# Kernel tuning notes

Measured on AMD Instinct MI355X. Metric: run time of the kernel, lower is better.

The kernel has to match this reference:

```python
import jax, jax.numpy as jnp
import numpy as np

N_TARGET = 1_000_000
GRID = 220
C_IN, C_OUT = 32, 64
BN_EPS = 1e-5


def _build_topology():
    # Real sparse-voxel topology: random occupied cells in a GRID^3 volume.
    rng = np.random.default_rng(0)
    raw = rng.integers(0, GRID, size=(1_400_000, 3), dtype=np.int64)
    keys = np.unique((raw[:, 0] * GRID + raw[:, 1]) * GRID + raw[:, 2])[:N_TARGET]
    N = keys.shape[0]
    coords = np.stack([keys // (GRID * GRID), (keys // GRID) % GRID, keys % GRID], axis=1)
    # Rulebook: for each of the 27 kernel offsets, index of the neighbor voxel (N = missing -> zero pad row).
    nbr = np.full((N, 27), N, dtype=np.int32)
    k = 0
    for dx in (-1, 0, 1):
        for dy in (-1, 0, 1):
            for dz in (-1, 0, 1):
                nc = coords + np.array([dx, dy, dz])
                valid = np.all((nc >= 0) & (nc < GRID), axis=1)
                nk = (nc[:, 0] * GRID + nc[:, 1]) * GRID + nc[:, 2]
                pos = np.clip(np.searchsorted(keys, nk), 0, N - 1)
                found = valid & (keys[pos] == nk)
                nbr[found, k] = pos[found].astype(np.int32)
                k += 1
    # MaxPool(2,2): voxels sharing coords//2 pool together.
    PG = GRID // 2 + 1
    pkeys = ((coords[:, 0] // 2) * PG + coords[:, 1] // 2) * PG + coords[:, 2] // 2
    uniq, pool_ids = np.unique(pkeys, return_inverse=True)
    return N, nbr, pool_ids.astype(np.int32), int(uniq.shape[0])


def setup_inputs() -> dict:
    N, nbr, pool_ids, num_pooled = _build_topology()
    key = jax.random.key(0)
    k1, k2, k3 = jax.random.split(key, 3)
    return {
        "feats": jax.random.normal(k1, (N, C_IN), dtype=jnp.float32),
        "W1": jax.random.normal(k2, (27, C_IN, C_OUT), dtype=jnp.float32) * 0.1,
        "gamma1": jnp.ones((C_OUT,), jnp.float32),
        "beta1": jnp.zeros((C_OUT,), jnp.float32),
        "W2": jax.random.normal(k3, (27, C_OUT, C_OUT), dtype=jnp.float32) * 0.1,
        "gamma2": jnp.ones((C_OUT,), jnp.float32),
        "beta2": jnp.zeros((C_OUT,), jnp.float32),
        "nbr_idx": jnp.asarray(nbr),
        "pool_ids": jnp.asarray(pool_ids),
        "num_pooled": num_pooled,
    }


def _sparse_conv3(f, W, nbr_idx):
    # f: [N, Cin], W: [27, Cin, Cout], nbr_idx: [N, 27] with pad index N.
    N = f.shape[0]
    fp = jnp.concatenate([f, jnp.zeros((1, f.shape[1]), f.dtype)], axis=0)  # zero pad row
    out = jnp.zeros((N, W.shape[2]), f.dtype)
    for k in range(27):  # fixed kernel offsets: gather -> GEMM -> accumulate
        out = out + fp[nbr_idx[:, k]] @ W[k]
    return out


def _batch_norm(f, gamma, beta):
    # Training-mode BN over the voxel dim (biased variance), as torch BatchNorm.
    m = f.mean(axis=0)
    v = f.var(axis=0)
    return (f - m) * jax.lax.rsqrt(v + BN_EPS) * gamma + beta


def reference(feats, W1, gamma1, beta1, W2, gamma2, beta2, nbr_idx, pool_ids, num_pooled):
    x = jax.nn.relu(_batch_norm(_sparse_conv3(feats, W1, nbr_idx), gamma1, beta1))
    x = _batch_norm(_sparse_conv3(x, W2, nbr_idx), gamma2, beta2)
    pooled = jax.ops.segment_max(x, pool_ids, num_segments=num_pooled)
    return x, pooled
```

## Files before the change

kernel.cpp:

```cpp
#include <hip/hip_runtime.h>
#include <hip/hip_bf16.h>
#include <stdint.h>

#define TPB 256

typedef __bf16 bf16x8 __attribute__((ext_vector_type(8)));
typedef float f32x4 __attribute__((ext_vector_type(4)));
union U16x8 { uint4 u; bf16x8 b; };

typedef const uint32_t __attribute__((address_space(1))) glb_u32;
typedef uint32_t __attribute__((address_space(3))) lds_u32;

__device__ __forceinline__ uint16_t f2bf_rne(float f) {
  union { float f; uint32_t u; } c; c.f = f;
  uint32_t r = 0x7FFFu + ((c.u >> 16) & 1u);
  return (uint16_t)((c.u + r) >> 16);
}

__global__ __launch_bounds__(TPB) void prep_w_kernel(
    const float* __restrict__ W1, const float* __restrict__ W2,
    uint16_t* __restrict__ w1t, uint16_t* __restrict__ w2t)
{
  int i = blockIdx.x * TPB + threadIdx.x;
  if (i < 27 * 2048) {
    int k = i >> 11, cin = (i >> 6) & 31, cout = i & 63;
    int cin2 = (((cin >> 3) ^ (cout & 3)) << 3) | (cin & 7);
    w1t[(k << 11) + (cout << 5) + cin2] = f2bf_rne(W1[i]);
  } else {
    int j = i - 27 * 2048;
    if (j < 27 * 4096) {
      int k = j >> 12, cin = (j >> 6) & 63, cout = j & 63;
      int cin2 = (((cin >> 3) ^ (cout & 7)) << 3) | (cin & 7);
      w2t[(k << 12) + (cout << 6) + cin2] = f2bf_rne(W2[j]);
    }
  }
}

__global__ __launch_bounds__(TPB) void prep_x0_kernel(
    const float* __restrict__ feats, uint16_t* __restrict__ x0, long long N)
{
  long long t = (long long)blockIdx.x * TPB + threadIdx.x;
  if (t >= (N + 1) * 4) return;
  long long e = t * 8;
  uint4 o;
  if (e < N * 32) {
    float4 a = *(const float4*)(feats + e);
    float4 b = *(const float4*)(feats + e + 4);
    o.x = (uint32_t)f2bf_rne(a.x) | ((uint32_t)f2bf_rne(a.y) << 16);
    o.y = (uint32_t)f2bf_rne(a.z) | ((uint32_t)f2bf_rne(a.w) << 16);
    o.z = (uint32_t)f2bf_rne(b.x) | ((uint32_t)f2bf_rne(b.y) << 16);
    o.w = (uint32_t)f2bf_rne(b.z) | ((uint32_t)f2bf_rne(b.w) << 16);
  } else {
    o.x = o.y = o.z = o.w = 0;
  }
  *(uint4*)(x0 + e) = o;
}

__global__ __launch_bounds__(TPB) void bucket_build_kernel(
    const int* __restrict__ pool_ids, int* __restrict__ count,
    int* __restrict__ members, long long N)
{
  long long i = (long long)blockIdx.x * TPB + threadIdx.x;
  if (i < N) {
    int pid = pool_ids[i];
    int slot = atomicAdd(&count[pid], 1);
    members[(long long)pid * 8 + slot] = (int)i;
  }
}

template <int CIN, int R>
__global__ __launch_bounds__(TPB, 2) void conv_mfma_kernel(
    const uint16_t* __restrict__ x, const uint16_t* __restrict__ wt,
    const int* __restrict__ nbr, float* __restrict__ y,
    float* __restrict__ statsrep, int N)
{
  constexpr int CHUNKS = CIN / 32;
  constexpr int LOGROWB = (CIN == 32) ? 6 : 7;
  constexpr int SWZ = (CIN == 32) ? 3 : 7;
  constexpr int WKB = 64 * CIN * 2;
  constexpr int NISSUE = WKB / (TPB * 16);
  constexpr int ROWS = 4 * R * 16;
  constexpr int NINTS = ROWS * 27;
  constexpr int NCH16 = NINTS / 4;

  __shared__ __align__(16) char Wlds[2][WKB];
  __shared__ __align__(16) int nbrLds[NINTS];
  __shared__ float sred[4][128];

  const int tid = threadIdx.x;
  const int lane = tid & 63;
  const int wave = tid >> 6;
  const int l15 = lane & 15;
  const int l4 = lane >> 4;
  const long long row0 = (long long)blockIdx.x * ROWS;

  f32x4 acc[R][4];
#pragma unroll
  for (int r = 0; r < R; ++r)
#pragma unroll
    for (int t = 0; t < 4; ++t)
      acc[r][t] = (f32x4){0.f, 0.f, 0.f, 0.f};

  {
    const char* nsrc = (const char*)nbr + row0 * 108;
    long long blkB = (long long)N * 108 - row0 * 108;
    int fullChunks = (int)(blkB >> 4);
    if (fullChunks > NCH16) fullChunks = NCH16;
#pragma unroll
    for (int u = 0; u < (NCH16 + TPB - 1) / TPB; ++u) {
      int idx = u * TPB + tid;
      if (idx < fullChunks)
        __builtin_amdgcn_global_load_lds((glb_u32*)(nsrc + idx * 16),
                                         (lds_u32*)((char*)nbrLds + idx * 16), 16, 0, 0);
    }
    for (int ii = fullChunks * 4 + tid; ii < NINTS; ii += TPB) {
      long long gi = row0 * 27 + ii;
      nbrLds[ii] = (gi < (long long)N * 27) ? nbr[gi] : N;
    }
  }

  auto stageW = [&](int k, int b) {
    const char* src = (const char*)(wt + (size_t)k * 64 * CIN);
#pragma unroll
    for (int u = 0; u < NISSUE; ++u) {
      int off = (tid + u * TPB) * 16;
      __builtin_amdgcn_global_load_lds((glb_u32*)(src + off),
                                       (lds_u32*)(&Wlds[b][off]), 16, 0, 0);
    }
  };
  auto gather = [&](int k, U16x8 (&dst)[R][CHUNKS]) {
#pragma unroll
    for (int r = 0; r < R; ++r) {
      int lrow = (wave * R + r) * 16 + l15;
      int g = nbrLds[lrow * 27 + k];
      const uint16_t* xr = x + (size_t)g * CIN + (l4 << 3);
#pragma unroll
      for (int c = 0; c < CHUNKS; ++c)
        dst[r][c].u = *(const uint4*)(xr + c * 32);
    }
  };
  auto compute = [&](int wsel, U16x8 (&xs)[R][CHUNKS]) {
    bf16x8 bfrag[4][CHUNKS];
#pragma unroll
    for (int t = 0; t < 4; ++t) {
      int n = t * 16 + l15;
#pragma unroll
      for (int c = 0; c < CHUNKS; ++c) {
        int colb = (l4 << 4) + (c << 6);
        int d = (n << LOGROWB) | (colb ^ ((n & SWZ) << 4));
        U16x8 tmp; tmp.u = *(const uint4*)(&Wlds[wsel][d]);
        bfrag[t][c] = tmp.b;
      }
    }
#pragma unroll
    for (int r = 0; r < R; ++r)
#pragma unroll
      for (int c = 0; c < CHUNKS; ++c)
#pragma unroll
        for (int t = 0; t < 4; ++t)
          acc[r][t] = __builtin_amdgcn_mfma_f32_16x16x32_bf16(
              xs[r][c].b, bfrag[t][c], acc[r][t], 0, 0, 0);
  };

  U16x8 xA[R][CHUNKS], xB[R][CHUNKS];

  stageW(0, 0);
  __syncthreads();
  gather(0, xA);

#pragma unroll 1
  for (int kk = 0; kk < 13; ++kk) {
    if (kk > 0) __syncthreads();
    stageW(2 * kk + 1, 1);
    gather(2 * kk + 1, xB);
    compute(0, xA);
    __syncthreads();
    if (2 * kk + 2 < 27) {
      stageW(2 * kk + 2, 0);
      gather(2 * kk + 2, xA);
    }
    compute(1, xB);
  }
  __syncthreads();
  compute(0, xA);

#pragma unroll
  for (int r = 0; r < R; ++r) {
    long long vr0 = row0 + (wave * R + r) * 16 + (l4 << 2);
#pragma unroll
    for (int reg = 0; reg < 4; ++reg) {
      long long vr = vr0 + reg;
      if (vr < N) {
        float* yr = y + vr * 64 + l15;
#pragma unroll
        for (int t = 0; t < 4; ++t) yr[t * 16] = acc[r][t][reg];
      }
    }
  }

  float s[4], s2[4];
#pragma unroll
  for (int t = 0; t < 4; ++t) { s[t] = 0.f; s2[t] = 0.f; }
#pragma unroll
  for (int r = 0; r < R; ++r) {
    long long vr0 = row0 + (wave * R + r) * 16 + (l4 << 2);
#pragma unroll
    for (int reg = 0; reg < 4; ++reg) {
      if (vr0 + reg < N) {
#pragma unroll
        for (int t = 0; t < 4; ++t) {
          float v = acc[r][t][reg];
          s[t] += v;
          s2[t] = fmaf(v, v, s2[t]);
        }
      }
    }
  }
#pragma unroll
  for (int t = 0; t < 4; ++t) {
    s[t] += __shfl_xor(s[t], 16);
    s[t] += __shfl_xor(s[t], 32);
    s2[t] += __shfl_xor(s2[t], 16);
    s2[t] += __shfl_xor(s2[t], 32);
  }
  __syncthreads();
  if (l4 == 0) {
#pragma unroll
    for (int t = 0; t < 4; ++t) {
      sred[wave][t * 16 + l15] = s[t];
      sred[wave][64 + t * 16 + l15] = s2[t];
    }
  }
  __syncthreads();
  if (tid < 128) {
    float tot = sred[0][tid] + sred[1][tid] + sred[2][tid] + sred[3][tid];
    atomicAdd(&statsrep[(blockIdx.x & 15) * 128 + tid], tot);
  }
}

__global__ void bn_finalize_kernel(const float* __restrict__ reps,
                                   float* __restrict__ fin, float n)
{
  int c = threadIdx.x;
  float s = 0.f, s2 = 0.f;
  for (int r = 0; r < 16; ++r) { s += reps[r * 128 + c]; s2 += reps[r * 128 + 64 + c]; }
  float mean = s / n;
  float var = s2 / n - mean * mean;
  fin[c] = mean;
  fin[64 + c] = rsqrtf(var + 1e-5f);
}

__global__ __launch_bounds__(TPB) void bn_relu_bf16_kernel(
    const float* __restrict__ y, const float* __restrict__ fin,
    const float* __restrict__ gamma, const float* __restrict__ beta,
    uint16_t* __restrict__ x1, long long N)
{
  long long e = ((long long)blockIdx.x * TPB + threadIdx.x) * 4;
  if (e >= (N + 1) * 64) return;
  long long row = e >> 6;
  int c = (int)(e & 63);
  ushort4 out;
  if (row < N) {
    float4 v = *(const float4*)(y + e);
    float4 m = *(const float4*)(fin + c);
    float4 r = *(const float4*)(fin + 64 + c);
    float4 g = *(const float4*)(gamma + c);
    float4 b = *(const float4*)(beta + c);
    float o0 = fmaf((v.x - m.x) * r.x, g.x, b.x);
    float o1 = fmaf((v.y - m.y) * r.y, g.y, b.y);
    float o2 = fmaf((v.z - m.z) * r.z, g.z, b.z);
    float o3 = fmaf((v.w - m.w) * r.w, g.w, b.w);
    o0 = o0 > 0.f ? o0 : 0.f; o1 = o1 > 0.f ? o1 : 0.f;
    o2 = o2 > 0.f ? o2 : 0.f; o3 = o3 > 0.f ? o3 : 0.f;
    out.x = f2bf_rne(o0); out.y = f2bf_rne(o1); out.z = f2bf_rne(o2); out.w = f2bf_rne(o3);
  } else {
    out.x = 0; out.y = 0; out.z = 0; out.w = 0;
  }
  *(ushort4*)(x1 + e) = out;
}

__global__ __launch_bounds__(TPB) void pool_max_kernel(
    const float* __restrict__ y, const float* __restrict__ fin,
    const float* __restrict__ gamma, const float* __restrict__ beta,
    const int* __restrict__ count, const int* __restrict__ members,
    float* __restrict__ pooled, long long P)
{
  long long pid = (long long)blockIdx.x * 16 + (threadIdx.x >> 4);
  if (pid >= P) return;
  int c0 = (threadIdx.x & 15) * 4;
  float4 m = *(const float4*)(fin + c0);
  float4 r = *(const float4*)(fin + 64 + c0);
  float4 g = *(const float4*)(gamma + c0);
  float4 b = *(const float4*)(beta + c0);
  int cnt = count[pid];
  float4 acc = {-3.4e38f, -3.4e38f, -3.4e38f, -3.4e38f};
  const int* mem = members + pid * 8;
  for (int t = 0; t < cnt; ++t) {
    long long row = mem[t];
    float4 v = *(const float4*)(y + row * 64 + c0);
    acc.x = fmaxf(acc.x, fmaf((v.x - m.x) * r.x, g.x, b.x));
    acc.y = fmaxf(acc.y, fmaf((v.y - m.y) * r.y, g.y, b.y));
    acc.z = fmaxf(acc.z, fmaf((v.z - m.z) * r.z, g.z, b.z));
    acc.w = fmaxf(acc.w, fmaf((v.w - m.w) * r.w, g.w, b.w));
  }
  *(float4*)(pooled + pid * 64 + c0) = acc;
}

__global__ __launch_bounds__(TPB) void bn_write_kernel(
    const float* __restrict__ y, const float* __restrict__ fin,
    const float* __restrict__ gamma, const float* __restrict__ beta,
    float* __restrict__ xout, long long N)
{
  long long e = ((long long)blockIdx.x * TPB + threadIdx.x) * 4;
  if (e >= N * 64) return;
  int c = (int)(e & 63);
  float4 v = *(const float4*)(y + e);
  float4 m = *(const float4*)(fin + c);
  float4 r = *(const float4*)(fin + 64 + c);
  float4 g = *(const float4*)(gamma + c);
  float4 b = *(const float4*)(beta + c);
  float4 o;
  o.x = fmaf((v.x - m.x) * r.x, g.x, b.x);
  o.y = fmaf((v.y - m.y) * r.y, g.y, b.y);
  o.z = fmaf((v.z - m.z) * r.z, g.z, b.z);
  o.w = fmaf((v.w - m.w) * r.w, g.w, b.w);
  *(float4*)(xout + e) = o;
}

extern "C" void kernel_launch(void* const* d_in, const int* in_sizes, int n_in,
                              void* d_out, int out_size, void* d_ws, size_t ws_size,
                              hipStream_t stream)
{
  const float* feats  = (const float*)d_in[0];
  const float* W1     = (const float*)d_in[1];
  const float* gamma1 = (const float*)d_in[2];
  const float* beta1  = (const float*)d_in[3];
  const float* W2     = (const float*)d_in[4];
  const float* gamma2 = (const float*)d_in[5];
  const float* beta2  = (const float*)d_in[6];
  const int* nbr      = (const int*)d_in[7];
  const int* pool_ids = (const int*)d_in[8];

  const long long N = (long long)in_sizes[0] / 32;
  const long long P = (long long)out_size / 64 - N;

  char* ws = (char*)d_ws;
  float* y = (float*)ws;
  size_t y_bytes = (size_t)N * 64 * 4;
  char* regB = ws + y_bytes;
  size_t regB_bytes = ((size_t)(N + 1) * 64 * 2 + 255) & ~(size_t)255;
  uint16_t* x0 = (uint16_t*)regB;
  uint16_t* x1 = (uint16_t*)regB;
  float* reps1 = (float*)(regB + regB_bytes);
  float* reps2 = reps1 + 16 * 128;
  float* fin1 = reps2 + 16 * 128;
  float* fin2 = fin1 + 128;

  float* xout = (float*)d_out;
  float* pooled = xout + (size_t)N * 64;
  int* count   = (int*)xout;
  int* members = count + P;
  uint16_t* w1t = (uint16_t*)pooled;
  uint16_t* w2t = w1t + 27 * 2048;

  hipMemsetAsync(reps1, 0, 2 * 16 * 128 * sizeof(float), stream);
  hipMemsetAsync(count, 0, (size_t)P * 4, stream);

  prep_w_kernel<<<(27 * 2048 + 27 * 4096 + TPB - 1) / TPB, TPB, 0, stream>>>(W1, W2, w1t, w2t);
  prep_x0_kernel<<<(int)(((N + 1) * 4 + TPB - 1) / TPB), TPB, 0, stream>>>(feats, x0, N);
  bucket_build_kernel<<<(int)((N + TPB - 1) / TPB), TPB, 0, stream>>>(pool_ids, count, members, N);

  const int convBlocks = (int)((N + 255) / 256);
  conv_mfma_kernel<32, 4><<<convBlocks, TPB, 0, stream>>>(x0, w1t, nbr, y, reps1, (int)N);
  bn_finalize_kernel<<<1, 64, 0, stream>>>(reps1, fin1, (float)N);

  long long e1 = ((N + 1) * 64) / 4;
  bn_relu_bf16_kernel<<<(int)((e1 + TPB - 1) / TPB), TPB, 0, stream>>>(
      y, fin1, gamma1, beta1, x1, N);

  conv_mfma_kernel<64, 4><<<convBlocks, TPB, 0, stream>>>(x1, w2t, nbr, y, reps2, (int)N);
  bn_finalize_kernel<<<1, 64, 0, stream>>>(reps2, fin2, (float)N);

  pool_max_kernel<<<(int)((P + 15) / 16), TPB, 0, stream>>>(
      y, fin2, gamma2, beta2, count, members, pooled, P);

  long long e2 = (N * 64) / 4;
  bn_write_kernel<<<(int)((e2 + TPB - 1) / TPB), TPB, 0, stream>>>(
      y, fin2, gamma2, beta2, xout, N);
}
```

Before: 758.9 us.

## Deepen conv pipeline with explicit vmcnt barriers, XCD-aware block remap, higher occupancy

Restructures the conv main loop so both weight buffers and both gather register sets are prefetched before the loop. Each stage then waits on a partial vmcnt plus a raw s_barrier instead of __syncthreads, with sched_barriers fencing the code, so gathers for the next offset stay in flight during MFMA compute. Block IDs are remapped so consecutive row ranges land on the same XCD for better L2 locality. Launch-bounds occupancy rises to 4 and 3 waves-per-SIMD targets, which risks register spills or correctness problems if the vmcnt count does not match the outstanding LDS-direct loads.

```diff
diff --git a/kernel.cpp b/kernel.cpp
--- a/kernel.cpp
+++ b/kernel.cpp
@@ -10,6 +10,16 @@
 
 typedef const uint32_t __attribute__((address_space(1))) glb_u32;
 typedef uint32_t __attribute__((address_space(3))) lds_u32;
+
+template <int N> __device__ __forceinline__ void wait_barrier() {
+  __builtin_amdgcn_sched_barrier(0);
+  asm volatile("s_waitcnt vmcnt(%0)" :: "i"(N) : "memory");
+  __builtin_amdgcn_s_barrier();
+  __builtin_amdgcn_sched_barrier(0);
+}
+__device__ __forceinline__ void fence_sched() {
+  __builtin_amdgcn_sched_barrier(0);
+}
 
 __device__ __forceinline__ uint16_t f2bf_rne(float f) {
   union { float f; uint32_t u; } c; c.f = f;
@@ -68,8 +78,8 @@
   }
 }
 
-template <int CIN, int R>
-__global__ __launch_bounds__(TPB, 2) void conv_mfma_kernel(
+template <int CIN, int R, int OCC>
+__global__ __launch_bounds__(TPB, OCC) void conv_mfma_kernel(
     const uint16_t* __restrict__ x, const uint16_t* __restrict__ wt,
     const int* __restrict__ nbr, float* __restrict__ y,
     float* __restrict__ statsrep, int N)
@@ -78,7 +88,8 @@
   constexpr int LOGROWB = (CIN == 32) ? 6 : 7;
   constexpr int SWZ = (CIN == 32) ? 3 : 7;
   constexpr int WKB = 64 * CIN * 2;
-  constexpr int NISSUE = WKB / (TPB * 16);
+  constexpr int NW = WKB / (TPB * 16);
+  constexpr int NG = R * CHUNKS;
   constexpr int ROWS = 4 * R * 16;
   constexpr int NINTS = ROWS * 27;
   constexpr int NCH16 = NINTS / 4;
@@ -92,7 +103,14 @@
   const int wave = tid >> 6;
   const int l15 = lane & 15;
   const int l4 = lane >> 4;
-  const long long row0 = (long long)blockIdx.x * ROWS;
+
+  int bid;
+  {
+    int nwg = gridDim.x, q = nwg >> 3, r = nwg & 7;
+    int xcd = blockIdx.x & 7, pos = blockIdx.x >> 3;
+    bid = (xcd < r ? xcd * (q + 1) : r * (q + 1) + (xcd - r) * q) + pos;
+  }
+  const long long row0 = (long long)bid * ROWS;
 
   f32x4 acc[R][4];
 #pragma unroll
@@ -122,7 +140,7 @@
   auto stageW = [&](int k, int b) {
     const char* src = (const char*)(wt + (size_t)k * 64 * CIN);
 #pragma unroll
-    for (int u = 0; u < NISSUE; ++u) {
+    for (int u = 0; u < NW; ++u) {
       int off = (tid + u * TPB) * 16;
       __builtin_amdgcn_global_load_lds((glb_u32*)(src + off),
                                        (lds_u32*)(&Wlds[b][off]), 16, 0, 0);
@@ -165,23 +183,29 @@
   U16x8 xA[R][CHUNKS], xB[R][CHUNKS];
 
   stageW(0, 0);
+  stageW(1, 1);
   __syncthreads();
   gather(0, xA);
+  gather(1, xB);
+  fence_sched();
 
 #pragma unroll 1
   for (int kk = 0; kk < 13; ++kk) {
-    if (kk > 0) __syncthreads();
-    stageW(2 * kk + 1, 1);
-    gather(2 * kk + 1, xB);
     compute(0, xA);
-    __syncthreads();
-    if (2 * kk + 2 < 27) {
-      stageW(2 * kk + 2, 0);
-      gather(2 * kk + 2, xA);
-    }
+    wait_barrier<NG>();
+    stageW(2 * kk + 2, 0);
+    fence_sched();
+    gather(2 * kk + 2, xA);
+    fence_sched();
     compute(1, xB);
-  }
-  __syncthreads();
+    wait_barrier<NG>();
+    if (kk < 12) {
+      stageW(2 * kk + 3, 1);
+      fence_sched();
+      gather(2 * kk + 3, xB);
+      fence_sched();
+    }
+  }
   compute(0, xA);
 
 #pragma unroll
@@ -234,7 +258,7 @@
   __syncthreads();
   if (tid < 128) {
     float tot = sred[0][tid] + sred[1][tid] + sred[2][tid] + sred[3][tid];
-    atomicAdd(&statsrep[(blockIdx.x & 15) * 128 + tid], tot);
+    atomicAdd(&statsrep[(bid & 15) * 128 + tid], tot);
   }
 }
 
@@ -371,14 +395,14 @@
   bucket_build_kernel<<<(int)((N + TPB - 1) / TPB), TPB, 0, stream>>>(pool_ids, count, members, N);
 
   const int convBlocks = (int)((N + 255) / 256);
-  conv_mfma_kernel<32, 4><<<convBlocks, TPB, 0, stream>>>(x0, w1t, nbr, y, reps1, (int)N);
+  conv_mfma_kernel<32, 4, 4><<<convBlocks, TPB, 0, stream>>>(x0, w1t, nbr, y, reps1, (int)N);
   bn_finalize_kernel<<<1, 64, 0, stream>>>(reps1, fin1, (float)N);
 
   long long e1 = ((N + 1) * 64) / 4;
   bn_relu_bf16_kernel<<<(int)((e1 + TPB - 1) / TPB), TPB, 0, stream>>>(
       y, fin1, gamma1, beta1, x1, N);
 
-  conv_mfma_kernel<64, 4><<<convBlocks, TPB, 0, stream>>>(x1, w2t, nbr, y, reps2, (int)N);
+  conv_mfma_kernel<64, 4, 3><<<convBlocks, TPB, 0, stream>>>(x1, w2t, nbr, y, reps2, (int)N);
   bn_finalize_kernel<<<1, 64, 0, stream>>>(reps2, fin2, (float)N);
 
   pool_max_kernel<<<(int)((P + 15) / 16), TPB, 0, stream>>>(
```

New measurement: 951.7 us. 25.4% more time.

## Store conv outputs as bf16, skip empty gather tiles, remap blocks per XCD

Applied to the files above, without the earlier changes.

The conv kernels now write their pre-BN output in bf16 instead of fp32, which halves the intermediate tensor's write and read traffic in the BN, pool and output kernels. Those consumers now read eight bf16 values per thread. The gather skips loads and MFMAs for 16-row tiles where no lane has a valid neighbor, which matters because the sparse volume leaves most neighbor slots empty. Block indices are remapped so contiguous row ranges land on the same XCD for L2 locality. Rounding pre-BN values to bf16 adds precision error to the final fp32 output, and BN statistics are still taken from fp32 accumulators, so they differ slightly from the stored values.

```diff
diff --git a/kernel.cpp b/kernel.cpp
--- a/kernel.cpp
+++ b/kernel.cpp
@@ -11,6 +11,9 @@
 typedef const uint32_t __attribute__((address_space(1))) glb_u32;
 typedef uint32_t __attribute__((address_space(3))) lds_u32;
 
+__device__ __forceinline__ float bfbits2f(uint32_t lo16) {
+  union { uint32_t u; float f; } c; c.u = lo16 << 16; return c.f;
+}
 __device__ __forceinline__ uint16_t f2bf_rne(float f) {
   union { float f; uint32_t u; } c; c.f = f;
   uint32_t r = 0x7FFFu + ((c.u >> 16) & 1u);
@@ -71,14 +74,14 @@
 template <int CIN, int R>
 __global__ __launch_bounds__(TPB, 2) void conv_mfma_kernel(
     const uint16_t* __restrict__ x, const uint16_t* __restrict__ wt,
-    const int* __restrict__ nbr, float* __restrict__ y,
+    const int* __restrict__ nbr, uint16_t* __restrict__ yb,
     float* __restrict__ statsrep, int N)
 {
   constexpr int CHUNKS = CIN / 32;
   constexpr int LOGROWB = (CIN == 32) ? 6 : 7;
   constexpr int SWZ = (CIN == 32) ? 3 : 7;
   constexpr int WKB = 64 * CIN * 2;
-  constexpr int NISSUE = WKB / (TPB * 16);
+  constexpr int NW = WKB / (TPB * 16);
   constexpr int ROWS = 4 * R * 16;
   constexpr int NINTS = ROWS * 27;
   constexpr int NCH16 = NINTS / 4;
@@ -92,7 +95,14 @@
   const int wave = tid >> 6;
   const int l15 = lane & 15;
   const int l4 = lane >> 4;
-  const long long row0 = (long long)blockIdx.x * ROWS;
+
+  int bid;
+  {
+    int nwg = gridDim.x, q = nwg >> 3, r = nwg & 7;
+    int xcd = blockIdx.x & 7, pos = blockIdx.x >> 3;
+    bid = (xcd < r ? xcd * (q + 1) : r * (q + 1) + (xcd - r) * q) + pos;
+  }
+  const long long row0 = (long long)bid * ROWS;
 
   f32x4 acc[R][4];
 #pragma unroll
@@ -122,24 +132,29 @@
   auto stageW = [&](int k, int b) {
     const char* src = (const char*)(wt + (size_t)k * 64 * CIN);
 #pragma unroll
-    for (int u = 0; u < NISSUE; ++u) {
+    for (int u = 0; u < NW; ++u) {
       int off = (tid + u * TPB) * 16;
       __builtin_amdgcn_global_load_lds((glb_u32*)(src + off),
                                        (lds_u32*)(&Wlds[b][off]), 16, 0, 0);
     }
   };
-  auto gather = [&](int k, U16x8 (&dst)[R][CHUNKS]) {
+  auto gather = [&](int k, U16x8 (&dst)[R][CHUNKS]) -> int {
+    int m = 0;
 #pragma unroll
     for (int r = 0; r < R; ++r) {
       int lrow = (wave * R + r) * 16 + l15;
       int g = nbrLds[lrow * 27 + k];
-      const uint16_t* xr = x + (size_t)g * CIN + (l4 << 3);
-#pragma unroll
-      for (int c = 0; c < CHUNKS; ++c)
-        dst[r][c].u = *(const uint4*)(xr + c * 32);
-    }
+      if (__any(g < N)) {
+        const uint16_t* xr = x + (size_t)g * CIN + (l4 << 3);
+#pragma unroll
+        for (int c = 0; c < CHUNKS; ++c)
+          dst[r][c].u = *(const uint4*)(xr + c * 32);
+        m |= 1 << r;
+      }
+    }
+    return m;
   };
-  auto compute = [&](int wsel, U16x8 (&xs)[R][CHUNKS]) {
+  auto compute = [&](int wsel, U16x8 (&xs)[R][CHUNKS], int mask) {
     bf16x8 bfrag[4][CHUNKS];
 #pragma unroll
     for (int t = 0; t < 4; ++t) {
@@ -153,36 +168,40 @@
       }
     }
 #pragma unroll
-    for (int r = 0; r < R; ++r)
-#pragma unroll
-      for (int c = 0; c < CHUNKS; ++c)
-#pragma unroll
-        for (int t = 0; t < 4; ++t)
-          acc[r][t] = __builtin_amdgcn_mfma_f32_16x16x32_bf16(
-              xs[r][c].b, bfrag[t][c], acc[r][t], 0, 0, 0);
+    for (int r = 0; r < R; ++r) {
+      if (mask & (1 << r)) {
+#pragma unroll
+        for (int c = 0; c < CHUNKS; ++c)
+#pragma unroll
+          for (int t = 0; t < 4; ++t)
+            acc[r][t] = __builtin_amdgcn_mfma_f32_16x16x32_bf16(
+                xs[r][c].b, bfrag[t][c], acc[r][t], 0, 0, 0);
+      }
+    }
   };
 
   U16x8 xA[R][CHUNKS], xB[R][CHUNKS];
+  int maskA, maskB;
 
   stageW(0, 0);
   __syncthreads();
-  gather(0, xA);
+  maskA = gather(0, xA);
 
 #pragma unroll 1
   for (int kk = 0; kk < 13; ++kk) {
     if (kk > 0) __syncthreads();
     stageW(2 * kk + 1, 1);
-    gather(2 * kk + 1, xB);
-    compute(0, xA);
+    maskB = gather(2 * kk + 1, xB);
+    compute(0, xA, maskA);
     __syncthreads();
     if (2 * kk + 2 < 27) {
       stageW(2 * kk + 2, 0);
-      gather(2 * kk + 2, xA);
-    }
-    compute(1, xB);
+      maskA = gather(2 * kk + 2, xA);
+    }
+    compute(1, xB, maskB);
   }
   __syncthreads();
-  compute(0, xA);
+  compute(0, xA, maskA);
 
 #pragma unroll
   for (int r = 0; r < R; ++r) {
@@ -191,9 +210,9 @@
     for (int reg = 0; reg < 4; ++reg) {
       long long vr = vr0 + reg;
       if (vr < N) {
-        float* yr = y + vr * 64 + l15;
-#pragma unroll
-        for (int t = 0; t < 4; ++t) yr[t * 16] = acc[r][t][reg];
+        uint16_t* yr = yb + vr * 64 + l15;
+#pragma unroll
+        for (int t = 0; t < 4; ++t) yr[t * 16] = f2bf_rne(acc[r][t][reg]);
       }
     }
   }
@@ -234,7 +253,7 @@
   __syncthreads();
   if (tid < 128) {
     float tot = sred[0][tid] + sred[1][tid] + sred[2][tid] + sred[3][tid];
-    atomicAdd(&statsrep[(blockIdx.x & 15) * 128 + tid], tot);
+    atomicAdd(&statsrep[(bid & 15) * 128 + tid], tot);
   }
 }
 
@@ -251,36 +270,39 @@
 }
 
 __global__ __launch_bounds__(TPB) void bn_relu_bf16_kernel(
-    const float* __restrict__ y, const float* __restrict__ fin,
+    const uint16_t* __restrict__ yb, const float* __restrict__ fin,
     const float* __restrict__ gamma, const float* __restrict__ beta,
     uint16_t* __restrict__ x1, long long N)
 {
-  long long e = ((long long)blockIdx.x * TPB + threadIdx.x) * 4;
+  long long e = ((long long)blockIdx.x * TPB + threadIdx.x) * 8;
   if (e >= (N + 1) * 64) return;
   long long row = e >> 6;
   int c = (int)(e & 63);
-  ushort4 out;
+  uint4 out;
   if (row < N) {
-    float4 v = *(const float4*)(y + e);
-    float4 m = *(const float4*)(fin + c);
-    float4 r = *(const float4*)(fin + 64 + c);
-    float4 g = *(const float4*)(gamma + c);
-    float4 b = *(const float4*)(beta + c);
-    float o0 = fmaf((v.x - m.x) * r.x, g.x, b.x);
-    float o1 = fmaf((v.y - m.y) * r.y, g.y, b.y);
-    float o2 = fmaf((v.z - m.z) * r.z, g.z, b.z);
-    float o3 = fmaf((v.w - m.w) * r.w, g.w, b.w);
-    o0 = o0 > 0.f ? o0 : 0.f; o1 = o1 > 0.f ? o1 : 0.f;
-    o2 = o2 > 0.f ? o2 : 0.f; o3 = o3 > 0.f ? o3 : 0.f;
-    out.x = f2bf_rne(o0); out.y = f2bf_rne(o1); out.z = f2bf_rne(o2); out.w = f2bf_rne(o3);
+    uint4 v = *(const uint4*)(yb + e);
+    const uint32_t vv[4] = {v.x, v.y, v.z, v.w};
+    uint32_t res[4];
+#pragma unroll
+    for (int q = 0; q < 4; ++q) {
+      int cc = c + q * 2;
+      float a0 = bfbits2f(vv[q] & 0xFFFFu);
+      float a1 = bfbits2f(vv[q] >> 16);
+      float o0 = fmaf((a0 - fin[cc]) * fin[64 + cc], gamma[cc], beta[cc]);
+      float o1 = fmaf((a1 - fin[cc + 1]) * fin[64 + cc + 1], gamma[cc + 1], beta[cc + 1]);
+      o0 = o0 > 0.f ? o0 : 0.f;
+      o1 = o1 > 0.f ? o1 : 0.f;
+      res[q] = (uint32_t)f2bf_rne(o0) | ((uint32_t)f2bf_rne(o1) << 16);
+    }
+    out.x = res[0]; out.y = res[1]; out.z = res[2]; out.w = res[3];
   } else {
-    out.x = 0; out.y = 0; out.z = 0; out.w = 0;
-  }
-  *(ushort4*)(x1 + e) = out;
+    out.x = out.y = out.z = out.w = 0;
+  }
+  *(uint4*)(x1 + e) = out;
 }
 
 __global__ __launch_bounds__(TPB) void pool_max_kernel(
-    const float* __restrict__ y, const float* __restrict__ fin,
+    const uint16_t* __restrict__ yb, const float* __restrict__ fin,
     const float* __restrict__ gamma, const float* __restrict__ beta,
     const int* __restrict__ count, const int* __restrict__ members,
     float* __restrict__ pooled, long long P)
@@ -297,34 +319,38 @@
   const int* mem = members + pid * 8;
   for (int t = 0; t < cnt; ++t) {
     long long row = mem[t];
-    float4 v = *(const float4*)(y + row * 64 + c0);
-    acc.x = fmaxf(acc.x, fmaf((v.x - m.x) * r.x, g.x, b.x));
-    acc.y = fmaxf(acc.y, fmaf((v.y - m.y) * r.y, g.y, b.y));
-    acc.z = fmaxf(acc.z, fmaf((v.z - m.z) * r.z, g.z, b.z));
-    acc.w = fmaxf(acc.w, fmaf((v.w - m.w) * r.w, g.w, b.w));
+    ushort4 v = *(const ushort4*)(yb + row * 64 + c0);
+    acc.x = fmaxf(acc.x, fmaf((bfbits2f(v.x) - m.x) * r.x, g.x, b.x));
+    acc.y = fmaxf(acc.y, fmaf((bfbits2f(v.y) - m.y) * r.y, g.y, b.y));
+    acc.z = fmaxf(acc.z, fmaf((bfbits2f(v.z) - m.z) * r.z, g.z, b.z));
+    acc.w = fmaxf(acc.w, fmaf((bfbits2f(v.w) - m.w) * r.w, g.w, b.w));
   }
   *(float4*)(pooled + pid * 64 + c0) = acc;
 }
 
 __global__ __launch_bounds__(TPB) void bn_write_kernel(
-    const float* __restrict__ y, const float* __restrict__ fin,
+    const uint16_t* __restrict__ yb, const float* __restrict__ fin,
     const float* __restrict__ gamma, const float* __restrict__ beta,
     float* __restrict__ xout, long long N)
 {
-  long long e = ((long long)blockIdx.x * TPB + threadIdx.x) * 4;
+  long long e = ((long long)blockIdx.x * TPB + threadIdx.x) * 8;
   if (e >= N * 64) return;
   int c = (int)(e & 63);
-  float4 v = *(const float4*)(y + e);
-  float4 m = *(const float4*)(fin + c);
-  float4 r = *(const float4*)(fin + 64 + c);
-  float4 g = *(const float4*)(gamma + c);
-  float4 b = *(const float4*)(beta + c);
-  float4 o;
-  o.x = fmaf((v.x - m.x) * r.x, g.x, b.x);
-  o.y = fmaf((v.y - m.y) * r.y, g.y, b.y);
-  o.z = fmaf((v.z - m.z) * r.z, g.z, b.z);
-  o.w = fmaf((v.w - m.w) * r.w, g.w, b.w);
-  *(float4*)(xout + e) = o;
+  uint4 v = *(const uint4*)(yb + e);
+  const uint32_t vv[4] = {v.x, v.y, v.z, v.w};
+  float o[8];
+#pragma unroll
+  for (int q = 0; q < 4; ++q) {
+    int cc = c + q * 2;
+    float a0 = bfbits2f(vv[q] & 0xFFFFu);
+    float a1 = bfbits2f(vv[q] >> 16);
+    o[q * 2 + 0] = fmaf((a0 - fin[cc]) * fin[64 + cc], gamma[cc], beta[cc]);
+    o[q * 2 + 1] = fmaf((a1 - fin[cc + 1]) * fin[64 + cc + 1], gamma[cc + 1], beta[cc + 1]);
+  }
+  float4 lo = {o[0], o[1], o[2], o[3]};
+  float4 hi = {o[4], o[5], o[6], o[7]};
+  *(float4*)(xout + e) = lo;
+  *(float4*)(xout + e + 4) = hi;
 }
 
 extern "C" void kernel_launch(void* const* d_in, const int* in_sizes, int n_in,
@@ -345,8 +371,8 @@
   const long long P = (long long)out_size / 64 - N;
 
   char* ws = (char*)d_ws;
-  float* y = (float*)ws;
-  size_t y_bytes = (size_t)N * 64 * 4;
+  uint16_t* yb = (uint16_t*)ws;
+  size_t y_bytes = ((size_t)N * 64 * 2 + 255) & ~(size_t)255;
   char* regB = ws + y_bytes;
   size_t regB_bytes = ((size_t)(N + 1) * 64 * 2 + 255) & ~(size_t)255;
   uint16_t* x0 = (uint16_t*)regB;
@@ -371,20 +397,20 @@
   bucket_build_kernel<<<(int)((N + TPB - 1) / TPB), TPB, 0, stream>>>(pool_ids, count, members, N);
 
   const int convBlocks = (int)((N + 255) / 256);
-  conv_mfma_kernel<32, 4><<<convBlocks, TPB, 0, stream>>>(x0, w1t, nbr, y, reps1, (int)N);
+  conv_mfma_kernel<32, 4><<<convBlocks, TPB, 0, stream>>>(x0, w1t, nbr, yb, reps1, (int)N);
   bn_finalize_kernel<<<1, 64, 0, stream>>>(reps1, fin1, (float)N);
 
-  long long e1 = ((N + 1) * 64) / 4;
-  bn_relu_bf16_kernel<<<(int)((e1 + TPB - 1) / TPB), TPB, 0, stream>>>(
-      y, fin1, gamma1, beta1, x1, N);
-
-  conv_mfma_kernel<64, 4><<<convBlocks, TPB, 0, stream>>>(x1, w2t, nbr, y, reps2, (int)N);
+  long long t1 = ((N + 1) * 64) / 8;
+  bn_relu_bf16_kernel<<<(int)((t1 + TPB - 1) / TPB), TPB, 0, stream>>>(
+      yb, fin1, gamma1, beta1, x1, N);
+
+  conv_mfma_kernel<64, 4><<<convBlocks, TPB, 0, stream>>>(x1, w2t, nbr, yb, reps2, (int)N);
   bn_finalize_kernel<<<1, 64, 0, stream>>>(reps2, fin2, (float)N);
 
   pool_max_kernel<<<(int)((P + 15) / 16), TPB, 0, stream>>>(
-      y, fin2, gamma2, beta2, count, members, pooled, P);
-
-  long long e2 = (N * 64) / 4;
-  bn_write_kernel<<<(int)((e2 + TPB - 1) / TPB), TPB, 0, stream>>>(
-      y, fin2, gamma2, beta2, xout, N);
-}
+      yb, fin2, gamma2, beta2, count, members, pooled, P);
+
+  long long t2 = (N * 64) / 8;
+  bn_write_kernel<<<(int)((t2 + TPB - 1) / TPB), TPB, 0, stream>>>(
+      yb, fin2, gamma2, beta2, xout, N);
+}
```

Measured after the change: 732.3 us. 3.5% less time.
